# Kernel optimization log

Measured on AMD Instinct MI355X. Metric: run time of the kernel, lower is better.

Reference implementation:

```python
import jax, jax.numpy as jnp
import numpy as np

N_HEAD = 16
T_THRESHOLD = 0.001


def setup_inputs() -> dict:
    key = jax.random.key(0)
    k_x, k_wa, k_ba, k_wp, k_bp = jax.random.split(key, 5)
    B, P, L, R = 8, 1024, 4, 256
    C = L * R  # n_embd = 1024
    s = 1.0 / np.sqrt(C)
    return {
        "x": jax.random.normal(k_x, (B, P, L, R), dtype=jnp.float32),
        "w_attn": jax.random.normal(k_wa, (C, 3 * C), dtype=jnp.float32) * s,
        "b_attn": jax.random.normal(k_ba, (3 * C,), dtype=jnp.float32) * 0.01,
        "w_proj": jax.random.normal(k_wp, (C, C), dtype=jnp.float32) * s,
        "b_proj": jax.random.normal(k_bp, (C,), dtype=jnp.float32) * 0.01,
    }


def reference(x, w_attn, b_attn, w_proj, b_proj):
    B, P, L, R = x.shape
    C = L * R
    H = N_HEAD
    hd = C // H
    xf = x.reshape(B, P, C)                      # (B, T, C)
    qkv = xf @ w_attn + b_attn                   # (B, T, 3C)
    q, k, v = jnp.split(qkv, 3, axis=-1)
    # (B, H, T, hd)
    q = q.reshape(B, P, H, hd).transpose(0, 2, 1, 3)
    k = k.reshape(B, P, H, hd).transpose(0, 2, 1, 3)
    v = v.reshape(B, P, H, hd).transpose(0, 2, 1, 3)
    att = jnp.einsum("bhqd,bhkd->bhqk", q, k) * (1.0 / np.sqrt(hd))
    att = jax.nn.softmax(att, axis=-1)
    att = jax.nn.relu(att - T_THRESHOLD)         # post-softmax thresholding
    y = jnp.einsum("bhqk,bhkd->bhqd", att, v)    # (B, H, T, hd)
    y = y.transpose(0, 2, 1, 3).reshape(B, P, C)
    y = y @ w_proj + b_proj
    return y.reshape(B, P, L, R)
```

## Files before the change

kernel.cpp:

```cpp
#include <hip/hip_runtime.h>


typedef _Float16 half8 __attribute__((ext_vector_type(8)));
typedef _Float16 half4_t __attribute__((ext_vector_type(4)));
typedef float floatx4 __attribute__((ext_vector_type(4)));

__device__ __forceinline__ void gl2lds16(const void* gsrc, void* lds) {
    __builtin_amdgcn_global_load_lds(
        (const __attribute__((address_space(1))) unsigned int*)gsrc,
        (__attribute__((address_space(3))) unsigned int*)lds,
        16, 0, 0);
}

__global__ __launch_bounds__(256) void conv_x(const float4* __restrict__ in,
                                              _Float16* __restrict__ out, int n4) {
    int idx = blockIdx.x * blockDim.x + threadIdx.x;
    int stride = gridDim.x * blockDim.x;
    for (int i = idx; i < n4; i += stride) {
        float4 v = in[i];
        half4_t h = { (_Float16)v.x, (_Float16)v.y, (_Float16)v.z, (_Float16)v.w };
        *(half4_t*)(out + (size_t)i * 4) = h;
    }
}

__global__ __launch_bounds__(256) void tconv(const float* __restrict__ in,
                                             _Float16* __restrict__ out, int R, int C) {
    __shared__ _Float16 t[64 * 65];
    int bx = blockIdx.x, by = blockIdx.y;
#pragma unroll
    for (int it = 0; it < 16; ++it) {
        int idx = it * 256 + threadIdx.x;
        int r = idx >> 6, c = idx & 63;
        t[c * 65 + r] = (_Float16)in[(size_t)(by * 64 + r) * C + bx * 64 + c];
    }
    __syncthreads();
#pragma unroll
    for (int it = 0; it < 16; ++it) {
        int idx = it * 256 + threadIdx.x;
        int rn = idx >> 6, ck = idx & 63;
        out[(size_t)(bx * 64 + rn) * R + by * 64 + ck] = t[rn * 65 + ck];
    }
}

__global__ __launch_bounds__(256) void pack_k(const _Float16* __restrict__ kn,
                                              _Float16* __restrict__ kP) {
    int cid = blockIdx.x * 256 + threadIdx.x;
    int lane = cid & 63, half = (cid >> 6) & 1, kb = (cid >> 7) & 63, bh = cid >> 13;
    int l15 = lane & 15, quad = lane >> 4;
    int b = bh >> 4, h = bh & 15;
    int t = kb * 16 + l15, d = half * 32 + quad * 8;
    half8 v = *(const half8*)(kn + (size_t)(b * 1024 + t) * 1024 + h * 64 + d);
    *(half8*)(kP + (size_t)cid * 8) = v;
}

__global__ __launch_bounds__(256) void pack_v(const _Float16* __restrict__ vn,
                                              _Float16* __restrict__ vP) {
    __shared__ _Float16 s[32][72];
    int kbv = blockIdx.x, bh = blockIdx.y;
    int b = bh >> 4, h = bh & 15;
    int tid = threadIdx.x;
    {
        int row = tid >> 3, piece = tid & 7;
        *(half8*)&s[row][piece * 8] =
            *(const half8*)(vn + (size_t)(b * 1024 + kbv * 32 + row) * 1024 + h * 64 + piece * 8);
    }
    __syncthreads();
    {
        int l15v = tid & 15, quad = (tid >> 4) & 3, cf = tid >> 6;
        half8 o;
#pragma unroll
        for (int j = 0; j < 8; ++j) o[j] = s[quad * 8 + j][cf * 16 + l15v];
        *(half8*)(vP + ((size_t)(bh * 32 + kbv) * 256 + tid) * 8) = o;
    }
}


#define GBAR __builtin_amdgcn_s_barrier()
#define WLGKM do { asm volatile("s_waitcnt lgkmcnt(0)" ::: "memory"); } while (0)
#define WVM2  do { asm volatile("s_waitcnt vmcnt(2)"   ::: "memory"); } while (0)

#define LDA(buf, rg)                                                                          \
    do {                                                                                      \
        _Pragma("unroll") for (int i = 0; i < 2; ++i) {                                       \
            int r_ = wm * 64 + ((rg) * 2 + i) * 16 + l15;                                     \
            _Pragma("unroll") for (int kk = 0; kk < 2; ++kk)                                  \
                a[i][kk] = *(const half8*)(sA + (buf) * 32768 + r_ * 128 +                    \
                                           ((((kk << 2) + quad) ^ (r_ & 7)) << 4));           \
        }                                                                                     \
    } while (0)

#define LDB(buf, cg, bb)                                                                      \
    do {                                                                                      \
        _Pragma("unroll") for (int j = 0; j < 2; ++j) {                                       \
            int r_ = wn * 64 + ((cg) * 2 + j) * 16 + l15;                                     \
            _Pragma("unroll") for (int kk = 0; kk < 2; ++kk)                                  \
                bb[j][kk] = *(const half8*)(sB + (buf) * 16384 + r_ * 128 +                   \
                                            ((((kk << 2) + quad) ^ (r_ & 7)) << 4));          \
        }                                                                                     \
    } while (0)

#define MMA(rg, cg, bb)                                                                       \
    do {                                                                                      \
        __builtin_amdgcn_s_setprio(1);                                                        \
        _Pragma("unroll") for (int kk = 0; kk < 2; ++kk)                                      \
            _Pragma("unroll") for (int i = 0; i < 2; ++i)                                     \
                _Pragma("unroll") for (int j = 0; j < 2; ++j)                                  \
                    acc[(rg) * 2 + i][(cg) * 2 + j] = __builtin_amdgcn_mfma_f32_16x16x32_f16( \
                        a[i][kk], bb[j][kk], acc[(rg) * 2 + i][(cg) * 2 + j], 0, 0, 0);       \
        __builtin_amdgcn_s_setprio(0);                                                        \
    } while (0)

template <bool SPLIT3>
__global__ __launch_bounds__(512, 2) void gemm8p(const _Float16* __restrict__ A,
                                                 const _Float16* __restrict__ BT,
                                                 const float* __restrict__ bias,
                                                 void* __restrict__ o0, void* __restrict__ o1,
                                                 void* __restrict__ o2, int N) {
    __shared__ __attribute__((aligned(16))) char lds[98304];
    char* sA = lds;
    char* sB = lds + 65536;
    int tid = threadIdx.x;
    int W = tid >> 6, lane = tid & 63, quad = lane >> 4, l15 = lane & 15;
    int wm = W >> 1, wn = W & 1;
    int m0 = blockIdx.y * 256, n0 = blockIdx.x * 128;

    auto stA = [&](int buf, int half, int k0) {
#pragma unroll
        for (int rnd = 0; rnd < 2; ++rnd) {
            int c = rnd * 512 + tid;
            int row = c >> 3;
            int q = (c & 7) ^ (row & 7);
            const _Float16* src = A + (size_t)(m0 + half * 128 + row) * 1024 + k0 + q * 8;
            int off = __builtin_amdgcn_readfirstlane(buf * 32768 + half * 16384 +
                                                     rnd * 8192 + (W << 10));
            gl2lds16(src, sA + off);
        }
    };
    auto stB = [&](int buf, int half, int k0) {
        int row = tid >> 3;
        int q = (tid & 7) ^ (row & 7);
        const _Float16* src = BT + (size_t)(n0 + half * 64 + row) * 1024 + k0 + q * 8;
        int off = __builtin_amdgcn_readfirstlane(buf * 16384 + half * 8192 + (W << 10));
        gl2lds16(src, sB + off);
    };

    half8 a[2][2], b0[2][2], b1[2][2];
    floatx4 acc[4][4] = {};

    stA(0, 0, 0); stA(0, 1, 0);
    stB(0, 0, 0); stB(0, 1, 0);
    stB(1, 0, 64); stB(1, 1, 64);
    WVM2;
    GBAR;

#pragma unroll 1
    for (int t = 0; t < 16; t += 2) {
        int k1 = (t + 1) << 6;
        int k2 = ((t + 2) & 15) << 6;
        int k3 = ((t + 3) & 15) << 6;
        LDA(0, 0); LDB(0, 0, b0); stA(1, 0, k1);
        GBAR; WLGKM; MMA(0, 0, b0); GBAR;
        LDB(0, 1, b1); stA(1, 1, k1);
        GBAR; WLGKM; MMA(0, 1, b1); GBAR;
        LDA(0, 1); stB(0, 0, k2);
        GBAR; WLGKM; MMA(1, 1, b1); GBAR;
        stB(0, 1, k2); WVM2;
        GBAR; WLGKM; MMA(1, 0, b0); GBAR;
        LDA(1, 0); LDB(1, 0, b0); stA(0, 0, k2);
        GBAR; WLGKM; MMA(0, 0, b0); GBAR;
        LDB(1, 1, b1); stA(0, 1, k2);
        GBAR; WLGKM; MMA(0, 1, b1); GBAR;
        LDA(1, 1); stB(1, 0, k3);
        GBAR; WLGKM; MMA(1, 1, b1); GBAR;
        stB(1, 1, k3); WVM2;
        GBAR; WLGKM; MMA(1, 0, b0); GBAR;
    }

    _Float16* hbase = nullptr;
    if (SPLIT3) {
        int sec = n0 >> 10;
        hbase = (_Float16*)(sec == 0 ? o0 : (sec == 1 ? o1 : o2));
    }
#pragma unroll
    for (int cf = 0; cf < 4; ++cf) {
        int gn = n0 + wn * 64 + cf * 16 + l15;
        float bv = bias[gn];
        int cn = gn & 1023;
#pragma unroll
        for (int rf = 0; rf < 4; ++rf) {
            int gmBase = m0 + wm * 64 + rf * 16 + quad * 4;
#pragma unroll
            for (int r = 0; r < 4; ++r) {
                float v = acc[rf][cf][r] + bv;
                if (SPLIT3) hbase[(size_t)(gmBase + r) * 1024 + cn] = (_Float16)v;
                else        ((float*)o0)[(size_t)(gmBase + r) * N + gn] = v;
            }
        }
    }
}

__device__ __forceinline__ int esw(int row, int colByte) {
    return row * 2048 + (colByte ^ ((row & 7) << 4));
}

__global__ __launch_bounds__(512, 4) void attn(const _Float16* __restrict__ qn,
                                               const _Float16* __restrict__ kP,
                                               const _Float16* __restrict__ vP,
                                               _Float16* __restrict__ y) {
    __shared__ __attribute__((aligned(16))) _Float16 E[32 * 1024];
    __shared__ float lsum[8][32];
    char* Eb = (char*)E;
    int tid = threadIdx.x;
    int W = tid >> 6, lane = tid & 63, quad = lane >> 4, l15 = lane & 15;
    int qt = blockIdx.x, bh = blockIdx.y;
    int b = bh >> 4, h = bh & 15;
    int q0 = qt * 32;

    half8 bq[2][2];
#pragma unroll
    for (int nf = 0; nf < 2; ++nf)
#pragma unroll
        for (int ks = 0; ks < 2; ++ks)
            bq[nf][ks] = *(const half8*)(qn + (size_t)(b * 1024 + q0 + nf * 16 + l15) * 1024 +
                                         h * 64 + ks * 32 + quad * 8);

    float lpart[2] = {0.f, 0.f};
#pragma unroll 4
    for (int mt = 0; mt < 8; ++mt) {
        int kb = W * 8 + mt;
        const _Float16* kp = kP + ((size_t)(bh * 64 + kb) * 128 + lane) * 8;
        half8 ak0 = *(const half8*)(kp);
        half8 ak1 = *(const half8*)(kp + 512);
#pragma unroll
        for (int nf = 0; nf < 2; ++nf) {
            floatx4 s = {};
            s = __builtin_amdgcn_mfma_f32_16x16x32_f16(ak0, bq[nf][0], s, 0, 0, 0);
            s = __builtin_amdgcn_mfma_f32_16x16x32_f16(ak1, bq[nf][1], s, 0, 0, 0);
            half4_t h4;
#pragma unroll
            for (int r = 0; r < 4; ++r) {
                float e = __expf(fminf(s[r] * 0.125f, 10.0f));
                lpart[nf] += e;
                h4[r] = (_Float16)e;
            }
            int q = nf * 16 + l15;
            int kbyte = (W * 128 + mt * 16 + quad * 4) * 2;
            *(half4_t*)(Eb + q * 2048 + (kbyte ^ ((q & 7) << 4))) = h4;
        }
    }
#pragma unroll
    for (int nf = 0; nf < 2; ++nf) {
        lpart[nf] += __shfl_xor(lpart[nf], 16);
        lpart[nf] += __shfl_xor(lpart[nf], 32);
    }
    if (lane < 16) {
        lsum[W][l15] = lpart[0];
        lsum[W][16 + l15] = lpart[1];
    }
    __syncthreads();

    half8 inv8[2], t8, z8;
#pragma unroll
    for (int j = 0; j < 8; ++j) { t8[j] = (_Float16)(-0.001f); z8[j] = (_Float16)0.f; }
#pragma unroll
    for (int rf = 0; rf < 2; ++rf) {
        float l = 0.f;
#pragma unroll
        for (int w = 0; w < 8; ++w) l += lsum[w][rf * 16 + l15];
        _Float16 invh = (_Float16)(1.0f / l);
#pragma unroll
        for (int j = 0; j < 8; ++j) inv8[rf][j] = invh;
    }

    floatx4 acc[2][4] = {};
#pragma unroll
    for (int kt = 0; kt < 4; ++kt) {
        int kk = W * 128 + kt * 32;
        half8 ap[2];
#pragma unroll
        for (int rf = 0; rf < 2; ++rf) {
            ap[rf] = *(const half8*)(Eb + esw(rf * 16 + l15, (kk + quad * 8) * 2));
            ap[rf] = ap[rf] * inv8[rf] + t8;
            ap[rf] = __builtin_elementwise_max(ap[rf], z8);
        }
        const _Float16* vbase = vP + ((size_t)(bh * 32 + (W * 4 + kt)) * 256 + lane) * 8;
        half8 bv[4];
#pragma unroll
        for (int cf = 0; cf < 4; ++cf)
            bv[cf] = *(const half8*)(vbase + cf * 512);
#pragma unroll
        for (int rf = 0; rf < 2; ++rf)
#pragma unroll
            for (int cf = 0; cf < 4; ++cf)
                acc[rf][cf] = __builtin_amdgcn_mfma_f32_16x16x32_f16(ap[rf], bv[cf], acc[rf][cf], 0, 0, 0);
    }
    __syncthreads();

    float* red = (float*)E;
#pragma unroll
    for (int rf = 0; rf < 2; ++rf)
#pragma unroll
        for (int cf = 0; cf < 4; ++cf)
#pragma unroll
            for (int r = 0; r < 4; ++r)
                red[W * 2048 + (rf * 16 + quad * 4 + r) * 64 + cf * 16 + l15] = acc[rf][cf][r];
    __syncthreads();
    {
        int e4 = tid * 4;
        int r = e4 >> 6, c = e4 & 63;
        floatx4 s = {};
#pragma unroll
        for (int w = 0; w < 8; ++w) s += *(const floatx4*)(red + w * 2048 + e4);
        half4_t hv = { (_Float16)s[0], (_Float16)s[1], (_Float16)s[2], (_Float16)s[3] };
        *(half4_t*)(y + (size_t)(b * 1024 + q0 + r) * 1024 + h * 64 + c) = hv;
    }
}

extern "C" void kernel_launch(void* const* d_in, const int* in_sizes, int n_in,
                              void* d_out, int out_size, void* d_ws, size_t ws_size,
                              hipStream_t stream) {
    const float* x  = (const float*)d_in[0];
    const float* wa = (const float*)d_in[1];
    const float* ba = (const float*)d_in[2];
    const float* wp = (const float*)d_in[3];
    const float* bp = (const float*)d_in[4];
    float* out = (float*)d_out;

    char* ws = (char*)d_ws;
    _Float16* xh  = (_Float16*)(ws);
    _Float16* vP  = (_Float16*)(ws);
    _Float16* qn  = (_Float16*)(ws + 16777216);
    _Float16* kn  = (_Float16*)(ws + 33554432);
    _Float16* y   = (_Float16*)(ws + 33554432);
    _Float16* vn  = (_Float16*)(ws + 50331648);
    _Float16* kP  = (_Float16*)(ws + 67108864);
    _Float16* waT = (_Float16*)(ws + 83886080);
    _Float16* wpT = (_Float16*)(ws + 90177536);

    conv_x<<<4096, 256, 0, stream>>>((const float4*)x, xh, 8388608 / 4);
    tconv<<<dim3(48, 16), 256, 0, stream>>>(wa, waT, 1024, 3072);
    tconv<<<dim3(16, 16), 256, 0, stream>>>(wp, wpT, 1024, 1024);
    gemm8p<true><<<dim3(24, 32), 512, 0, stream>>>(xh, waT, ba, (void*)qn, (void*)kn, (void*)vn, 3072);
    pack_k<<<4096, 256, 0, stream>>>(kn, kP);
    pack_v<<<dim3(32, 128), 256, 0, stream>>>(vn, vP);
    attn<<<dim3(32, 128), 512, 0, stream>>>(qn, kP, vP, y);
    gemm8p<false><<<dim3(8, 32), 512, 0, stream>>>(y, wpT, bp, (void*)out, nullptr, nullptr, 1024);
}
```

Measured before the change: 280.3 us.

## Halve attention query tile to 16 rows to raise occupancy

The attention kernel now handles 16 query rows per block instead of 32. This halves the LDS score buffer and the register accumulators, doubles the grid, and raises the launch-bounds occupancy hint from 4 to 8. The exponential is switched to a native exp2 with a pre-scaled log2e constant, and the cross-wave reduction buffer is padded to a stride of 68 to avoid bank conflicts. In exchange, each K and V fragment is now loaded twice as often across blocks, and fewer MFMA operations are done per load.

```diff
diff --git a/kernel.cpp b/kernel.cpp
--- a/kernel.cpp
+++ b/kernel.cpp
@@ -3,7 +3,9 @@
 
 typedef _Float16 half8 __attribute__((ext_vector_type(8)));
 typedef _Float16 half4_t __attribute__((ext_vector_type(4)));
+typedef _Float16 half2_t __attribute__((ext_vector_type(2)));
 typedef float floatx4 __attribute__((ext_vector_type(4)));
+typedef float floatx2 __attribute__((ext_vector_type(2)));
 
 __device__ __forceinline__ void gl2lds16(const void* gsrc, void* lds) {
     __builtin_amdgcn_global_load_lds(
@@ -203,116 +205,94 @@
     return row * 2048 + (colByte ^ ((row & 7) << 4));
 }
 
-__global__ __launch_bounds__(512, 4) void attn(const _Float16* __restrict__ qn,
+__global__ __launch_bounds__(512, 8) void attn(const _Float16* __restrict__ qn,
                                                const _Float16* __restrict__ kP,
                                                const _Float16* __restrict__ vP,
                                                _Float16* __restrict__ y) {
-    __shared__ __attribute__((aligned(16))) _Float16 E[32 * 1024];
-    __shared__ float lsum[8][32];
-    char* Eb = (char*)E;
+    __shared__ __attribute__((aligned(16))) char smem[34816];
+    __shared__ float lsum[8][16];
+    char* Eb = smem;
     int tid = threadIdx.x;
     int W = tid >> 6, lane = tid & 63, quad = lane >> 4, l15 = lane & 15;
     int qt = blockIdx.x, bh = blockIdx.y;
     int b = bh >> 4, h = bh & 15;
-    int q0 = qt * 32;
-
-    half8 bq[2][2];
-#pragma unroll
-    for (int nf = 0; nf < 2; ++nf)
-#pragma unroll
-        for (int ks = 0; ks < 2; ++ks)
-            bq[nf][ks] = *(const half8*)(qn + (size_t)(b * 1024 + q0 + nf * 16 + l15) * 1024 +
-                                         h * 64 + ks * 32 + quad * 8);
-
-    float lpart[2] = {0.f, 0.f};
+    int q0 = qt * 16;
+
+    half8 bq[2];
+#pragma unroll
+    for (int ks = 0; ks < 2; ++ks)
+        bq[ks] = *(const half8*)(qn + (size_t)(b * 1024 + q0 + l15) * 1024 +
+                                 h * 64 + ks * 32 + quad * 8);
+
+    float lpart = 0.f;
 #pragma unroll 4
     for (int mt = 0; mt < 8; ++mt) {
         int kb = W * 8 + mt;
         const _Float16* kp = kP + ((size_t)(bh * 64 + kb) * 128 + lane) * 8;
         half8 ak0 = *(const half8*)(kp);
         half8 ak1 = *(const half8*)(kp + 512);
-#pragma unroll
-        for (int nf = 0; nf < 2; ++nf) {
-            floatx4 s = {};
-            s = __builtin_amdgcn_mfma_f32_16x16x32_f16(ak0, bq[nf][0], s, 0, 0, 0);
-            s = __builtin_amdgcn_mfma_f32_16x16x32_f16(ak1, bq[nf][1], s, 0, 0, 0);
-            half4_t h4;
-#pragma unroll
-            for (int r = 0; r < 4; ++r) {
-                float e = __expf(fminf(s[r] * 0.125f, 10.0f));
-                lpart[nf] += e;
-                h4[r] = (_Float16)e;
-            }
-            int q = nf * 16 + l15;
-            int kbyte = (W * 128 + mt * 16 + quad * 4) * 2;
-            *(half4_t*)(Eb + q * 2048 + (kbyte ^ ((q & 7) << 4))) = h4;
+        floatx4 s = {};
+        s = __builtin_amdgcn_mfma_f32_16x16x32_f16(ak0, bq[0], s, 0, 0, 0);
+        s = __builtin_amdgcn_mfma_f32_16x16x32_f16(ak1, bq[1], s, 0, 0, 0);
+        half4_t h4;
+#pragma unroll
+        for (int r = 0; r < 4; ++r) {
+            float e = __builtin_amdgcn_exp2f(fminf(s[r] * 0.18033688f, 14.4269504f));
+            lpart += e;
+            h4[r] = (_Float16)e;
         }
-    }
-#pragma unroll
-    for (int nf = 0; nf < 2; ++nf) {
-        lpart[nf] += __shfl_xor(lpart[nf], 16);
-        lpart[nf] += __shfl_xor(lpart[nf], 32);
-    }
-    if (lane < 16) {
-        lsum[W][l15] = lpart[0];
-        lsum[W][16 + l15] = lpart[1];
-    }
-    __syncthreads();
-
-    half8 inv8[2], t8, z8;
+        int kbyte = (W * 128 + mt * 16 + quad * 4) * 2;
+        *(half4_t*)(Eb + l15 * 2048 + (kbyte ^ ((l15 & 7) << 4))) = h4;
+    }
+    lpart += __shfl_xor(lpart, 16);
+    lpart += __shfl_xor(lpart, 32);
+    if (lane < 16) lsum[W][l15] = lpart;
+    __syncthreads();
+
+    half8 inv8, t8, z8;
 #pragma unroll
     for (int j = 0; j < 8; ++j) { t8[j] = (_Float16)(-0.001f); z8[j] = (_Float16)0.f; }
-#pragma unroll
-    for (int rf = 0; rf < 2; ++rf) {
+    {
         float l = 0.f;
 #pragma unroll
-        for (int w = 0; w < 8; ++w) l += lsum[w][rf * 16 + l15];
+        for (int w = 0; w < 8; ++w) l += lsum[w][l15];
         _Float16 invh = (_Float16)(1.0f / l);
 #pragma unroll
-        for (int j = 0; j < 8; ++j) inv8[rf][j] = invh;
-    }
-
-    floatx4 acc[2][4] = {};
+        for (int j = 0; j < 8; ++j) inv8[j] = invh;
+    }
+
+    floatx4 acc[4] = {};
 #pragma unroll
     for (int kt = 0; kt < 4; ++kt) {
         int kk = W * 128 + kt * 32;
-        half8 ap[2];
-#pragma unroll
-        for (int rf = 0; rf < 2; ++rf) {
-            ap[rf] = *(const half8*)(Eb + esw(rf * 16 + l15, (kk + quad * 8) * 2));
-            ap[rf] = ap[rf] * inv8[rf] + t8;
-            ap[rf] = __builtin_elementwise_max(ap[rf], z8);
-        }
+        half8 ap = *(const half8*)(Eb + esw(l15, (kk + quad * 8) * 2));
+        ap = ap * inv8 + t8;
+        ap = __builtin_elementwise_max(ap, z8);
         const _Float16* vbase = vP + ((size_t)(bh * 32 + (W * 4 + kt)) * 256 + lane) * 8;
         half8 bv[4];
 #pragma unroll
         for (int cf = 0; cf < 4; ++cf)
             bv[cf] = *(const half8*)(vbase + cf * 512);
 #pragma unroll
-        for (int rf = 0; rf < 2; ++rf)
-#pragma unroll
-            for (int cf = 0; cf < 4; ++cf)
-                acc[rf][cf] = __builtin_amdgcn_mfma_f32_16x16x32_f16(ap[rf], bv[cf], acc[rf][cf], 0, 0, 0);
-    }
-    __syncthreads();
-
-    float* red = (float*)E;
-#pragma unroll
-    for (int rf = 0; rf < 2; ++rf)
-#pragma unroll
         for (int cf = 0; cf < 4; ++cf)
-#pragma unroll
-            for (int r = 0; r < 4; ++r)
-                red[W * 2048 + (rf * 16 + quad * 4 + r) * 64 + cf * 16 + l15] = acc[rf][cf][r];
+            acc[cf] = __builtin_amdgcn_mfma_f32_16x16x32_f16(ap, bv[cf], acc[cf], 0, 0, 0);
+    }
+    __syncthreads();
+
+    float* red = (float*)smem;
+#pragma unroll
+    for (int cf = 0; cf < 4; ++cf)
+#pragma unroll
+        for (int r = 0; r < 4; ++r)
+            red[W * 1088 + (quad * 4 + r) * 68 + cf * 16 + l15] = acc[cf][r];
     __syncthreads();
     {
-        int e4 = tid * 4;
-        int r = e4 >> 6, c = e4 & 63;
-        floatx4 s = {};
-#pragma unroll
-        for (int w = 0; w < 8; ++w) s += *(const floatx4*)(red + w * 2048 + e4);
-        half4_t hv = { (_Float16)s[0], (_Float16)s[1], (_Float16)s[2], (_Float16)s[3] };
-        *(half4_t*)(y + (size_t)(b * 1024 + q0 + r) * 1024 + h * 64 + c) = hv;
+        int r = tid >> 5, c = (tid & 31) * 2;
+        floatx2 s = {};
+#pragma unroll
+        for (int w = 0; w < 8; ++w) s += *(const floatx2*)(red + w * 1088 + r * 68 + c);
+        half2_t hv = { (_Float16)s[0], (_Float16)s[1] };
+        *(half2_t*)(y + (size_t)(b * 1024 + q0 + r) * 1024 + h * 64 + c) = hv;
     }
 }
 
@@ -343,6 +323,6 @@
     gemm8p<true><<<dim3(24, 32), 512, 0, stream>>>(xh, waT, ba, (void*)qn, (void*)kn, (void*)vn, 3072);
     pack_k<<<4096, 256, 0, stream>>>(kn, kP);
     pack_v<<<dim3(32, 128), 256, 0, stream>>>(vn, vP);
-    attn<<<dim3(32, 128), 512, 0, stream>>>(qn, kP, vP, y);
+    attn<<<dim3(64, 128), 512, 0, stream>>>(qn, kP, vP, y);
     gemm8p<false><<<dim3(8, 32), 512, 0, stream>>>(y, wpT, bp, (void*)out, nullptr, nullptr, 1024);
 }
```

Result: slower. 291.2 us (+3.9%).

## Split attention keys across sixteen waves per block with two-stage LDS reduction

Applied to the files above, without the earlier changes.

The attention kernel grows from 512 to 1024 threads per block, so each wave covers half as many key tiles in both the QK^T/exp phase and the PV phase. The cross-wave partial sums are reduced in two stages: the upper eight waves store to LDS, then the lower eight waves add in place. Block indices are also swizzled to change the order in which (batch, head, query-tile) blocks are scheduled, and exp is computed with the exp2 builtin using a prescaled constant. The goal is more parallelism and shorter per-wave latency per tile, at the cost of an extra barrier, a read-modify-write reduction, and tighter register budgets under the new launch bounds.

```diff
diff --git a/kernel.cpp b/kernel.cpp
--- a/kernel.cpp
+++ b/kernel.cpp
@@ -3,7 +3,9 @@
 
 typedef _Float16 half8 __attribute__((ext_vector_type(8)));
 typedef _Float16 half4_t __attribute__((ext_vector_type(4)));
+typedef _Float16 half2_t __attribute__((ext_vector_type(2)));
 typedef float floatx4 __attribute__((ext_vector_type(4)));
+typedef float floatx2 __attribute__((ext_vector_type(2)));
 
 __device__ __forceinline__ void gl2lds16(const void* gsrc, void* lds) {
     __builtin_amdgcn_global_load_lds(
@@ -203,16 +205,18 @@
     return row * 2048 + (colByte ^ ((row & 7) << 4));
 }
 
-__global__ __launch_bounds__(512, 4) void attn(const _Float16* __restrict__ qn,
-                                               const _Float16* __restrict__ kP,
-                                               const _Float16* __restrict__ vP,
-                                               _Float16* __restrict__ y) {
+__global__ __launch_bounds__(1024, 8) void attn(const _Float16* __restrict__ qn,
+                                                const _Float16* __restrict__ kP,
+                                                const _Float16* __restrict__ vP,
+                                                _Float16* __restrict__ y) {
     __shared__ __attribute__((aligned(16))) _Float16 E[32 * 1024];
-    __shared__ float lsum[8][32];
+    __shared__ float lsum[16][32];
     char* Eb = (char*)E;
     int tid = threadIdx.x;
     int W = tid >> 6, lane = tid & 63, quad = lane >> 4, l15 = lane & 15;
-    int qt = blockIdx.x, bh = blockIdx.y;
+    int flat = blockIdx.y * 32 + blockIdx.x;
+    int swz = (flat & 7) * 512 + (flat >> 3);
+    int qt = swz & 31, bh = swz >> 5;
     int b = bh >> 4, h = bh & 15;
     int q0 = qt * 32;
 
@@ -225,9 +229,9 @@
                                          h * 64 + ks * 32 + quad * 8);
 
     float lpart[2] = {0.f, 0.f};
-#pragma unroll 4
-    for (int mt = 0; mt < 8; ++mt) {
-        int kb = W * 8 + mt;
+#pragma unroll
+    for (int mt = 0; mt < 4; ++mt) {
+        int kb = W * 4 + mt;
         const _Float16* kp = kP + ((size_t)(bh * 64 + kb) * 128 + lane) * 8;
         half8 ak0 = *(const half8*)(kp);
         half8 ak1 = *(const half8*)(kp + 512);
@@ -239,12 +243,12 @@
             half4_t h4;
 #pragma unroll
             for (int r = 0; r < 4; ++r) {
-                float e = __expf(fminf(s[r] * 0.125f, 10.0f));
+                float e = __builtin_amdgcn_exp2f(fminf(s[r] * 0.18033688f, 14.4269504f));
                 lpart[nf] += e;
                 h4[r] = (_Float16)e;
             }
             int q = nf * 16 + l15;
-            int kbyte = (W * 128 + mt * 16 + quad * 4) * 2;
+            int kbyte = (W * 64 + mt * 16 + quad * 4) * 2;
             *(half4_t*)(Eb + q * 2048 + (kbyte ^ ((q & 7) << 4))) = h4;
         }
     }
@@ -266,7 +270,7 @@
     for (int rf = 0; rf < 2; ++rf) {
         float l = 0.f;
 #pragma unroll
-        for (int w = 0; w < 8; ++w) l += lsum[w][rf * 16 + l15];
+        for (int w = 0; w < 16; ++w) l += lsum[w][rf * 16 + l15];
         _Float16 invh = (_Float16)(1.0f / l);
 #pragma unroll
         for (int j = 0; j < 8; ++j) inv8[rf][j] = invh;
@@ -274,8 +278,8 @@
 
     floatx4 acc[2][4] = {};
 #pragma unroll
-    for (int kt = 0; kt < 4; ++kt) {
-        int kk = W * 128 + kt * 32;
+    for (int kt = 0; kt < 2; ++kt) {
+        int kk = W * 64 + kt * 32;
         half8 ap[2];
 #pragma unroll
         for (int rf = 0; rf < 2; ++rf) {
@@ -283,7 +287,7 @@
             ap[rf] = ap[rf] * inv8[rf] + t8;
             ap[rf] = __builtin_elementwise_max(ap[rf], z8);
         }
-        const _Float16* vbase = vP + ((size_t)(bh * 32 + (W * 4 + kt)) * 256 + lane) * 8;
+        const _Float16* vbase = vP + ((size_t)(bh * 32 + (W * 2 + kt)) * 256 + lane) * 8;
         half8 bv[4];
 #pragma unroll
         for (int cf = 0; cf < 4; ++cf)
@@ -297,22 +301,37 @@
     __syncthreads();
 
     float* red = (float*)E;
-#pragma unroll
-    for (int rf = 0; rf < 2; ++rf)
-#pragma unroll
-        for (int cf = 0; cf < 4; ++cf)
-#pragma unroll
-            for (int r = 0; r < 4; ++r)
-                red[W * 2048 + (rf * 16 + quad * 4 + r) * 64 + cf * 16 + l15] = acc[rf][cf][r];
+    if (W >= 8) {
+#pragma unroll
+        for (int rf = 0; rf < 2; ++rf)
+#pragma unroll
+            for (int cf = 0; cf < 4; ++cf)
+#pragma unroll
+                for (int r = 0; r < 4; ++r)
+                    red[(W - 8) * 2048 + (rf * 16 + quad * 4 + r) * 64 + cf * 16 + l15] =
+                        acc[rf][cf][r];
+    }
+    __syncthreads();
+    if (W < 8) {
+#pragma unroll
+        for (int rf = 0; rf < 2; ++rf)
+#pragma unroll
+            for (int cf = 0; cf < 4; ++cf)
+#pragma unroll
+                for (int r = 0; r < 4; ++r) {
+                    int idx = W * 2048 + (rf * 16 + quad * 4 + r) * 64 + cf * 16 + l15;
+                    red[idx] += acc[rf][cf][r];
+                }
+    }
     __syncthreads();
     {
-        int e4 = tid * 4;
-        int r = e4 >> 6, c = e4 & 63;
-        floatx4 s = {};
-#pragma unroll
-        for (int w = 0; w < 8; ++w) s += *(const floatx4*)(red + w * 2048 + e4);
-        half4_t hv = { (_Float16)s[0], (_Float16)s[1], (_Float16)s[2], (_Float16)s[3] };
-        *(half4_t*)(y + (size_t)(b * 1024 + q0 + r) * 1024 + h * 64 + c) = hv;
+        int e2 = tid * 2;
+        int r = e2 >> 6, c = e2 & 63;
+        floatx2 s = {};
+#pragma unroll
+        for (int w = 0; w < 8; ++w) s += *(const floatx2*)(red + w * 2048 + e2);
+        half2_t hv = { (_Float16)s[0], (_Float16)s[1] };
+        *(half2_t*)(y + (size_t)(b * 1024 + q0 + r) * 1024 + h * 64 + c) = hv;
     }
 }
 
@@ -343,6 +362,6 @@
     gemm8p<true><<<dim3(24, 32), 512, 0, stream>>>(xh, waT, ba, (void*)qn, (void*)kn, (void*)vn, 3072);
     pack_k<<<4096, 256, 0, stream>>>(kn, kP);
     pack_v<<<dim3(32, 128), 256, 0, stream>>>(vn, vP);
-    attn<<<dim3(32, 128), 512, 0, stream>>>(qn, kP, vP, y);
+    attn<<<dim3(32, 128), 1024, 0, stream>>>(qn, kP, vP, y);
     gemm8p<false><<<dim3(8, 32), 512, 0, stream>>>(y, wpT, bp, (void*)out, nullptr, nullptr, 1024);
 }
```

Result: slower. 298.4 us (+6.5%).

## Fuse K/V packing into QKV GEMM epilogue via LDS staging, swizzle attention blocks

Applied to the files above, without the earlier changes.

The QKV GEMM epilogue now stages its output tile in LDS and writes Q row-major, K in the packed kP layout and V in the transposed vP layout directly, so the separate pack_k and pack_v kernels and their extra global round trips go away. Stores become 16-byte vectors instead of scattered half stores. The attention grid index is also remapped so consecutive workgroups spread across heads and batches, which may change cache locality. The cost is a longer epilogue with an extra barrier and reuse of the GEMM's LDS buffer after waiting for all outstanding loads.

```diff
diff --git a/kernel.cpp b/kernel.cpp
--- a/kernel.cpp
+++ b/kernel.cpp
@@ -42,42 +42,11 @@
     }
 }
 
-__global__ __launch_bounds__(256) void pack_k(const _Float16* __restrict__ kn,
-                                              _Float16* __restrict__ kP) {
-    int cid = blockIdx.x * 256 + threadIdx.x;
-    int lane = cid & 63, half = (cid >> 6) & 1, kb = (cid >> 7) & 63, bh = cid >> 13;
-    int l15 = lane & 15, quad = lane >> 4;
-    int b = bh >> 4, h = bh & 15;
-    int t = kb * 16 + l15, d = half * 32 + quad * 8;
-    half8 v = *(const half8*)(kn + (size_t)(b * 1024 + t) * 1024 + h * 64 + d);
-    *(half8*)(kP + (size_t)cid * 8) = v;
-}
-
-__global__ __launch_bounds__(256) void pack_v(const _Float16* __restrict__ vn,
-                                              _Float16* __restrict__ vP) {
-    __shared__ _Float16 s[32][72];
-    int kbv = blockIdx.x, bh = blockIdx.y;
-    int b = bh >> 4, h = bh & 15;
-    int tid = threadIdx.x;
-    {
-        int row = tid >> 3, piece = tid & 7;
-        *(half8*)&s[row][piece * 8] =
-            *(const half8*)(vn + (size_t)(b * 1024 + kbv * 32 + row) * 1024 + h * 64 + piece * 8);
-    }
-    __syncthreads();
-    {
-        int l15v = tid & 15, quad = (tid >> 4) & 3, cf = tid >> 6;
-        half8 o;
-#pragma unroll
-        for (int j = 0; j < 8; ++j) o[j] = s[quad * 8 + j][cf * 16 + l15v];
-        *(half8*)(vP + ((size_t)(bh * 32 + kbv) * 256 + tid) * 8) = o;
-    }
-}
-
 
 #define GBAR __builtin_amdgcn_s_barrier()
 #define WLGKM do { asm volatile("s_waitcnt lgkmcnt(0)" ::: "memory"); } while (0)
 #define WVM2  do { asm volatile("s_waitcnt vmcnt(2)"   ::: "memory"); } while (0)
+#define WVM0  do { asm volatile("s_waitcnt vmcnt(0)"   ::: "memory"); } while (0)
 
 #define LDA(buf, rg)                                                                          \
     do {                                                                                      \
@@ -176,24 +145,97 @@
         GBAR; WLGKM; MMA(1, 0, b0); GBAR;
     }
 
-    _Float16* hbase = nullptr;
-    if (SPLIT3) {
+    if constexpr (!SPLIT3) {
+#pragma unroll
+        for (int cf = 0; cf < 4; ++cf) {
+            int gn = n0 + wn * 64 + cf * 16 + l15;
+            float bv = bias[gn];
+#pragma unroll
+            for (int rf = 0; rf < 4; ++rf) {
+                int gmBase = m0 + wm * 64 + rf * 16 + quad * 4;
+#pragma unroll
+                for (int r = 0; r < 4; ++r)
+                    ((float*)o0)[(size_t)(gmBase + r) * N + gn] = acc[rf][cf][r] + bv;
+            }
+        }
+    } else {
+        WVM0;
+        GBAR;
         int sec = n0 >> 10;
-        hbase = (_Float16*)(sec == 0 ? o0 : (sec == 1 ? o1 : o2));
-    }
-#pragma unroll
-    for (int cf = 0; cf < 4; ++cf) {
-        int gn = n0 + wn * 64 + cf * 16 + l15;
-        float bv = bias[gn];
-        int cn = gn & 1023;
-#pragma unroll
-        for (int rf = 0; rf < 4; ++rf) {
-            int gmBase = m0 + wm * 64 + rf * 16 + quad * 4;
-#pragma unroll
-            for (int r = 0; r < 4; ++r) {
-                float v = acc[rf][cf][r] + bv;
-                if (SPLIT3) hbase[(size_t)(gmBase + r) * 1024 + cn] = (_Float16)v;
-                else        ((float*)o0)[(size_t)(gmBase + r) * N + gn] = v;
+        int nb = n0 & 1023;
+        int b = m0 >> 10;
+        int tb = m0 & 1023;
+        _Float16* qno = (_Float16*)o0;
+        _Float16* kPo = (_Float16*)o1;
+        _Float16* vPo = (_Float16*)o2;
+        if (sec == 2) {
+#pragma unroll
+            for (int cf = 0; cf < 4; ++cf) {
+                int n = wn * 64 + cf * 16 + l15;
+                float bv = bias[n0 + n];
+#pragma unroll
+                for (int rf = 0; rf < 4; ++rf) {
+                    int m = wm * 64 + rf * 16 + quad * 4;
+                    half4_t h4;
+#pragma unroll
+                    for (int r = 0; r < 4; ++r) h4[r] = (_Float16)(acc[rf][cf][r] + bv);
+                    *(half4_t*)(lds + n * 528 + ((m >> 3) << 4) + (m & 7) * 2) = h4;
+                }
+            }
+            __syncthreads();
+            int l15v = tid & 15;
+            int moct = W * 4 + ((tid >> 4) & 3);
+            int t = tb + moct * 8;
+            int kbv = (t >> 5) & 31, quad_v = (t >> 3) & 3;
+#pragma unroll
+            for (int i = 0; i < 8; ++i) {
+                int hh = i >> 2, cf = i & 3;
+                int n = hh * 64 + cf * 16 + l15v;
+                half8 v = *(const half8*)(lds + n * 528 + (moct << 4));
+                int gcol = nb + n;
+                int h = gcol >> 6, d = gcol & 63;
+                size_t chunk = (size_t)((b * 16 + h) * 32 + kbv) * 256 +
+                               (d >> 4) * 64 + quad_v * 16 + (d & 15);
+                *(half8*)(vPo + chunk * 8) = v;
+            }
+        } else {
+#pragma unroll
+            for (int cf = 0; cf < 4; ++cf) {
+                int n = wn * 64 + cf * 16 + l15;
+                float bv = bias[n0 + n];
+                int nbyte = ((n >> 3) << 4) + (n & 7) * 2;
+#pragma unroll
+                for (int rf = 0; rf < 4; ++rf) {
+                    int m = wm * 64 + rf * 16 + quad * 4;
+#pragma unroll
+                    for (int r = 0; r < 4; ++r)
+                        *(_Float16*)(lds + (m + r) * 272 + nbyte) =
+                            (_Float16)(acc[rf][cf][r] + bv);
+                }
+            }
+            __syncthreads();
+            if (sec == 0) {
+                int noct = tid & 15;
+#pragma unroll
+                for (int i = 0; i < 8; ++i) {
+                    int m = i * 32 + (tid >> 4);
+                    half8 v = *(const half8*)(lds + m * 272 + (noct << 4));
+                    *(half8*)(qno + (size_t)(b * 1024 + tb + m) * 1024 + nb + noct * 8) = v;
+                }
+            } else {
+                int l15k = tid & 15, noct = (tid >> 4) & 15;
+#pragma unroll
+                for (int i = 0; i < 8; ++i) {
+                    int mb = i * 2 + (tid >> 8);
+                    int m = mb * 16 + l15k;
+                    half8 v = *(const half8*)(lds + m * 272 + (noct << 4));
+                    int gcol = nb + noct * 8;
+                    int h = gcol >> 6, d0 = gcol & 63;
+                    int t = tb + m;
+                    size_t chunk = (size_t)((b * 16 + h) * 64 + (t >> 4)) * 128 +
+                                   (d0 >> 5) * 64 + ((d0 >> 3) & 3) * 16 + l15k;
+                    *(half8*)(kPo + chunk * 8) = v;
+                }
             }
         }
     }
@@ -212,7 +254,9 @@
     char* Eb = (char*)E;
     int tid = threadIdx.x;
     int W = tid >> 6, lane = tid & 63, quad = lane >> 4, l15 = lane & 15;
-    int qt = blockIdx.x, bh = blockIdx.y;
+    int flat = blockIdx.y * 32 + blockIdx.x;
+    int swz = (flat & 7) * 512 + (flat >> 3);
+    int qt = swz & 31, bh = swz >> 5;
     int b = bh >> 4, h = bh & 15;
     int q0 = qt * 32;
 
@@ -327,22 +371,18 @@
     float* out = (float*)d_out;
 
     char* ws = (char*)d_ws;
-    _Float16* xh  = (_Float16*)(ws);
-    _Float16* vP  = (_Float16*)(ws);
+    _Float16* y   = (_Float16*)(ws);
     _Float16* qn  = (_Float16*)(ws + 16777216);
-    _Float16* kn  = (_Float16*)(ws + 33554432);
-    _Float16* y   = (_Float16*)(ws + 33554432);
-    _Float16* vn  = (_Float16*)(ws + 50331648);
-    _Float16* kP  = (_Float16*)(ws + 67108864);
-    _Float16* waT = (_Float16*)(ws + 83886080);
-    _Float16* wpT = (_Float16*)(ws + 90177536);
+    _Float16* kP  = (_Float16*)(ws + 33554432);
+    _Float16* vP  = (_Float16*)(ws + 50331648);
+    _Float16* waT = (_Float16*)(ws + 67108864);
+    _Float16* wpT = (_Float16*)(ws + 73400320);
+    _Float16* xh  = (_Float16*)(ws + 75497472);
 
     conv_x<<<4096, 256, 0, stream>>>((const float4*)x, xh, 8388608 / 4);
     tconv<<<dim3(48, 16), 256, 0, stream>>>(wa, waT, 1024, 3072);
     tconv<<<dim3(16, 16), 256, 0, stream>>>(wp, wpT, 1024, 1024);
-    gemm8p<true><<<dim3(24, 32), 512, 0, stream>>>(xh, waT, ba, (void*)qn, (void*)kn, (void*)vn, 3072);
-    pack_k<<<4096, 256, 0, stream>>>(kn, kP);
-    pack_v<<<dim3(32, 128), 256, 0, stream>>>(vn, vP);
+    gemm8p<true><<<dim3(24, 32), 512, 0, stream>>>(xh, waT, ba, (void*)qn, (void*)kP, (void*)vP, 3072);
     attn<<<dim3(32, 128), 512, 0, stream>>>(qn, kP, vP, y);
     gemm8p<false><<<dim3(8, 32), 512, 0, stream>>>(y, wpT, bp, (void*)out, nullptr, nullptr, 1024);
 }
```

After: 260.2 us. -7.2%, faster.
